# Kernel tuning notes

Hardware: AMD Instinct MI355X
Metric: run time of the kernel (lower is better)

Reference implementation:

```python
import jax, jax.numpy as jnp
import numpy as np

# Module config (matches init_kwargs)
T, B, C = 2048, 8, 1024   # seq_len, batch, input_size
H, K = 16, 31             # num_heads, kernel_size
PAD_L = 30                # padding_l (causal)


def setup_inputs() -> dict:
    key = jax.random.key(0)
    k1, k2 = jax.random.split(key)
    x = jax.random.normal(k1, (T, B, C), dtype=jnp.float32)
    # nn.Parameter(num_heads, kernel_size), xavier-init approximated by randn
    weight = jax.random.normal(k2, (H, K), dtype=jnp.float32)
    return {"x": x, "weight": weight}


def reference(x, weight):
    # x: (T, B, C); weight: (H, K)
    # weight_softmax=True: softmax over kernel taps per head
    w = jax.nn.softmax(weight, axis=-1)  # (H, K)
    # permute to (B, C, T) as the CUDA kernel expects
    x_bct = jnp.transpose(x, (1, 2, 0))
    # expand per-head kernel to per-channel depthwise kernel: (C, 1, K)
    w_ck = jnp.repeat(w, C // H, axis=0)[:, None, :]
    # lightconv: out[b,c,t] = sum_k w[head(c),k] * x_pad[b,c,t+k],
    # left pad = PAD_L, right pad = K-1-PAD_L (causal when PAD_L=K-1).
    # conv_general_dilated is cross-correlation, matching the CUDA kernel.
    out = jax.lax.conv_general_dilated(
        x_bct, w_ck,
        window_strides=(1,),
        padding=[(PAD_L, K - 1 - PAD_L)],
        dimension_numbers=("NCH", "OIH", "NCH"),
        feature_group_count=C,
    )  # (B, C, T)
    # bias=False, so just permute back to (T, B, C)
    return jnp.transpose(out, (2, 0, 1))
```

## Files before the change

### kernel.cpp

```cpp
#include <hip/hip_runtime.h>
#include <math.h>
#include <stdint.h>

#define T_LEN 2048
#define B_SZ  8
#define C_SZ  1024
#define NH    16
#define KW    31
#define HALO  (KW - 1)
#define BLOCK 256
#define CG    256
#define TT    16
#define CHUNK 128
#define NTILE (CHUNK / TT)
#define RING  64
#define WIN   (TT + HALO)
#define ROWSTRIDE (B_SZ * C_SZ)

#define GLOBAL_AS(p) ((const __attribute__((address_space(1))) void*)(p))
#define LDS_AS(p)    ((__attribute__((address_space(3))) void*)(p))

__global__ __launch_bounds__(BLOCK, 2) void lightconv_kernel(
    const float* __restrict__ x, const float* __restrict__ weight,
    float* __restrict__ out) {
  __shared__ float ring[RING][CG];
  __shared__ float sw[NH][KW];

  const int tid  = threadIdx.x;
  const int wave = tid >> 6;
  const int lane = tid & 63;

  const int cg = blockIdx.x & 3;
  const int tc = blockIdx.x >> 2;
  const int b  = blockIdx.y;
  const int c0 = cg * CG;
  const int tb = tc * CHUNK;

  if (tid < NH) {
    float wv[KW];
    float m = -1e30f;
#pragma unroll
    for (int k = 0; k < KW; ++k) {
      wv[k] = weight[tid * KW + k];
      m = fmaxf(m, wv[k]);
    }
    float s = 0.f;
#pragma unroll
    for (int k = 0; k < KW; ++k) {
      wv[k] = expf(wv[k] - m);
      s += wv[k];
    }
    const float inv = 1.f / s;
#pragma unroll
    for (int k = 0; k < KW; ++k) sw[tid][k] = wv[k] * inv;
  }

  const float* xbase = x + (size_t)b * C_SZ + c0;
#pragma unroll
  for (int rr = 0; rr < 12; ++rr) {
    const int idx = wave + rr * 4;
    if (idx < WIN) {
      const int t = tb - HALO + idx;
      if (t >= 0) {
        const int slot = (t + 2048) & (RING - 1);
        const float* gp = xbase + (size_t)t * ROWSTRIDE + lane * 4;
        __builtin_amdgcn_global_load_lds(GLOBAL_AS(gp), LDS_AS(&ring[slot][0]),
                                         16, 0, 0);
      }
    }
  }
  if (tb == 0) {
#pragma unroll
    for (int i = 0; i < HALO; ++i) {
      ring[(i - HALO + 2048) & (RING - 1)][tid] = 0.f;
    }
  }
  __syncthreads();

  const int head = (c0 >> 6) + wave;
  float wk[KW];
#pragma unroll
  for (int k = 0; k < KW; ++k) {
    wk[k] = __uint_as_float(
        __builtin_amdgcn_readfirstlane(__float_as_uint(sw[head][k])));
  }

  for (int j = 0; j < NTILE; ++j) {
    const int tstart = tb + j * TT;

    if (j + 1 < NTILE) {
#pragma unroll
      for (int rr = 0; rr < TT / 4; ++rr) {
        const int t = tstart + TT + wave + rr * 4;
        const int slot = t & (RING - 1);
        const float* gp = xbase + (size_t)t * ROWSTRIDE + lane * 4;
        __builtin_amdgcn_global_load_lds(GLOBAL_AS(gp), LDS_AS(&ring[slot][0]),
                                         16, 0, 0);
      }
      asm volatile("s_waitcnt vmcnt(4)" ::: "memory");
    } else {
      asm volatile("s_waitcnt vmcnt(0)" ::: "memory");
    }
    __builtin_amdgcn_s_barrier();
    __builtin_amdgcn_sched_barrier(0);

    float xv[WIN];
#pragma unroll
    for (int i = 0; i < WIN; ++i) {
      const int t = tstart - HALO + i;
      xv[i] = ring[(t + 2048) & (RING - 1)][tid];
    }
    float* op = out + ((size_t)tstart * B_SZ + b) * C_SZ + c0 + tid;
#pragma unroll
    for (int o = 0; o < TT; ++o) {
      float a = 0.f;
#pragma unroll
      for (int k = 0; k < KW; ++k) a = fmaf(wk[k], xv[o + k], a);
      op[(size_t)o * ROWSTRIDE] = a;
    }

    __builtin_amdgcn_s_barrier();
    __builtin_amdgcn_sched_barrier(0);
  }
}

extern "C" void kernel_launch(void* const* d_in, const int* in_sizes, int n_in,
                              void* d_out, int out_size, void* d_ws, size_t ws_size,
                              hipStream_t stream) {
  const float* x = (const float*)d_in[0];
  const float* w = (const float*)d_in[1];
  float* out = (float*)d_out;
  (void)in_sizes; (void)n_in; (void)out_size; (void)d_ws; (void)ws_size;

  dim3 grid((T_LEN / CHUNK) * (C_SZ / CG), B_SZ);
  dim3 block(BLOCK);
  lightconv_kernel<<<grid, block, 0, stream>>>(x, w, out);
}
```

Measured before the change: 35.59 us.

## Use single-wave blocks per head with barrier-free ring buffer and per-lane softmax

Shrinks each block from four waves covering 256 channels to one 64-lane wave covering one head's 64 channels. This lets all block-wide barriers go and replaces them with per-wave vmcnt waits tuned to the order of loads and stores. Each lane now computes the head's softmax directly instead of staging it through shared memory. Async global-to-LDS loads drop from 16-byte to 4-byte per lane, which issues more load instructions in exchange for a grid of four times as many smaller blocks, possibly giving better occupancy and latency hiding.

```diff
diff --git a/kernel.cpp b/kernel.cpp
--- a/kernel.cpp
+++ b/kernel.cpp
@@ -1,6 +1,5 @@
 #include <hip/hip_runtime.h>
 #include <math.h>
-#include <stdint.h>
 
 #define T_LEN 2048
 #define B_SZ  8
@@ -8,8 +7,6 @@
 #define NH    16
 #define KW    31
 #define HALO  (KW - 1)
-#define BLOCK 256
-#define CG    256
 #define TT    16
 #define CHUNK 128
 #define NTILE (CHUNK / TT)
@@ -20,97 +17,91 @@
 #define GLOBAL_AS(p) ((const __attribute__((address_space(1))) void*)(p))
 #define LDS_AS(p)    ((__attribute__((address_space(3))) void*)(p))
 
-__global__ __launch_bounds__(BLOCK, 2) void lightconv_kernel(
+__global__ __launch_bounds__(64, 2) void lightconv_kernel(
     const float* __restrict__ x, const float* __restrict__ weight,
     float* __restrict__ out) {
-  __shared__ float ring[RING][CG];
-  __shared__ float sw[NH][KW];
+  __shared__ float ring[RING][64];
+  const int lane = threadIdx.x;
 
-  const int tid  = threadIdx.x;
-  const int wave = tid >> 6;
-  const int lane = tid & 63;
+  const int cgrp = blockIdx.x & 15;
+  const int tc   = blockIdx.x >> 4;
+  const int b    = blockIdx.y;
+  const int c0   = cgrp * 64;
+  const int tb   = tc * CHUNK;
 
-  const int cg = blockIdx.x & 3;
-  const int tc = blockIdx.x >> 2;
-  const int b  = blockIdx.y;
-  const int c0 = cg * CG;
-  const int tb = tc * CHUNK;
-
-  if (tid < NH) {
-    float wv[KW];
-    float m = -1e30f;
+  float wv[KW];
+  float m = -1e30f;
 #pragma unroll
-    for (int k = 0; k < KW; ++k) {
-      wv[k] = weight[tid * KW + k];
-      m = fmaxf(m, wv[k]);
-    }
-    float s = 0.f;
+  for (int k = 0; k < KW; ++k) {
+    wv[k] = weight[cgrp * KW + k];
+    m = fmaxf(m, wv[k]);
+  }
+  float s = 0.f;
 #pragma unroll
-    for (int k = 0; k < KW; ++k) {
-      wv[k] = expf(wv[k] - m);
-      s += wv[k];
-    }
-    const float inv = 1.f / s;
-#pragma unroll
-    for (int k = 0; k < KW; ++k) sw[tid][k] = wv[k] * inv;
+  for (int k = 0; k < KW; ++k) {
+    wv[k] = expf(wv[k] - m);
+    s += wv[k];
   }
-
-  const float* xbase = x + (size_t)b * C_SZ + c0;
-#pragma unroll
-  for (int rr = 0; rr < 12; ++rr) {
-    const int idx = wave + rr * 4;
-    if (idx < WIN) {
-      const int t = tb - HALO + idx;
-      if (t >= 0) {
-        const int slot = (t + 2048) & (RING - 1);
-        const float* gp = xbase + (size_t)t * ROWSTRIDE + lane * 4;
-        __builtin_amdgcn_global_load_lds(GLOBAL_AS(gp), LDS_AS(&ring[slot][0]),
-                                         16, 0, 0);
-      }
-    }
-  }
-  if (tb == 0) {
-#pragma unroll
-    for (int i = 0; i < HALO; ++i) {
-      ring[(i - HALO + 2048) & (RING - 1)][tid] = 0.f;
-    }
-  }
-  __syncthreads();
-
-  const int head = (c0 >> 6) + wave;
+  const float inv = 1.f / s;
   float wk[KW];
 #pragma unroll
   for (int k = 0; k < KW; ++k) {
     wk[k] = __uint_as_float(
-        __builtin_amdgcn_readfirstlane(__float_as_uint(sw[head][k])));
+        __builtin_amdgcn_readfirstlane(__float_as_uint(wv[k] * inv)));
   }
 
+  const float* xbase = x + (size_t)b * C_SZ + c0;
+
+  if (tb == 0) {
+#pragma unroll
+    for (int i = 0; i < HALO; ++i) {
+      ring[(2048 - HALO + i) & (RING - 1)][lane] = 0.f;
+    }
+#pragma unroll
+    for (int i = 0; i < TT; ++i) {
+      const float* gp = xbase + (size_t)i * ROWSTRIDE + lane;
+      __builtin_amdgcn_global_load_lds(GLOBAL_AS(gp),
+                                       LDS_AS(&ring[i & (RING - 1)][0]), 4, 0, 0);
+    }
+  } else {
+#pragma unroll
+    for (int i = 0; i < WIN; ++i) {
+      const int t = tb - HALO + i;
+      const float* gp = xbase + (size_t)t * ROWSTRIDE + lane;
+      __builtin_amdgcn_global_load_lds(GLOBAL_AS(gp),
+                                       LDS_AS(&ring[(t + 2048) & (RING - 1)][0]),
+                                       4, 0, 0);
+    }
+  }
+
+#pragma unroll 1
   for (int j = 0; j < NTILE; ++j) {
     const int tstart = tb + j * TT;
 
     if (j + 1 < NTILE) {
 #pragma unroll
-      for (int rr = 0; rr < TT / 4; ++rr) {
-        const int t = tstart + TT + wave + rr * 4;
-        const int slot = t & (RING - 1);
-        const float* gp = xbase + (size_t)t * ROWSTRIDE + lane * 4;
-        __builtin_amdgcn_global_load_lds(GLOBAL_AS(gp), LDS_AS(&ring[slot][0]),
-                                         16, 0, 0);
+      for (int r = 0; r < TT; ++r) {
+        const int t = tstart + TT + r;
+        const float* gp = xbase + (size_t)t * ROWSTRIDE + lane;
+        __builtin_amdgcn_global_load_lds(GLOBAL_AS(gp),
+                                         LDS_AS(&ring[(t + 2048) & (RING - 1)][0]),
+                                         4, 0, 0);
       }
-      asm volatile("s_waitcnt vmcnt(4)" ::: "memory");
+    }
+    if (j == 0 || j == NTILE - 1) {
+      asm volatile("s_waitcnt vmcnt(16)" ::: "memory");
     } else {
-      asm volatile("s_waitcnt vmcnt(0)" ::: "memory");
+      asm volatile("s_waitcnt vmcnt(31)" ::: "memory");
     }
-    __builtin_amdgcn_s_barrier();
     __builtin_amdgcn_sched_barrier(0);
 
     float xv[WIN];
 #pragma unroll
     for (int i = 0; i < WIN; ++i) {
       const int t = tstart - HALO + i;
-      xv[i] = ring[(t + 2048) & (RING - 1)][tid];
+      xv[i] = ring[(t + 2048) & (RING - 1)][lane];
     }
-    float* op = out + ((size_t)tstart * B_SZ + b) * C_SZ + c0 + tid;
+    float* op = out + ((size_t)tstart * B_SZ + b) * C_SZ + c0 + lane;
 #pragma unroll
     for (int o = 0; o < TT; ++o) {
       float a = 0.f;
@@ -118,9 +109,6 @@
       for (int k = 0; k < KW; ++k) a = fmaf(wk[k], xv[o + k], a);
       op[(size_t)o * ROWSTRIDE] = a;
     }
-
-    __builtin_amdgcn_s_barrier();
-    __builtin_amdgcn_sched_barrier(0);
   }
 }
 
@@ -132,7 +120,7 @@
   float* out = (float*)d_out;
   (void)in_sizes; (void)n_in; (void)out_size; (void)d_ws; (void)ws_size;
 
-  dim3 grid((T_LEN / CHUNK) * (C_SZ / CG), B_SZ);
-  dim3 block(BLOCK);
+  dim3 grid((C_SZ / 64) * (T_LEN / CHUNK), B_SZ);
+  dim3 block(64);
   lightconv_kernel<<<grid, block, 0, stream>>>(x, w, out);
 }
```

Measured after the change: 33.48 us. -5.9%, faster.
